# Optimization experiments

Hardware: AMD Instinct MI355X
Metric: run time of the kernel (lower is better)

Reference implementation:

```python
import jax, jax.numpy as jnp
import numpy as np
from math import ceil

N, C_IN, HV, WV = 4, 3, 256, 256
C, K, NUM_LAYERS = 16, 3, 10
HK, WK = 45, 45
PROX_SCALE, KSCALE, KBSCALE, EPS = 10.0, 100.0, 0.01, 1e-8


def conv2_same(x, w):
    # torch F.conv2d (cross-correlation) with 'same' padding
    return jax.lax.conv_general_dilated(x, w, (1, 1), 'SAME',
                                        dimension_numbers=('NCHW', 'OIHW', 'NCHW'))


def pad_to(x, size):
    h, w = x.shape[-2], x.shape[-1]
    pads = [(0, 0)] * (x.ndim - 2) + [(0, size[0] - h), (0, size[1] - w)]
    return jnp.pad(x, pads)


def soft_threshold(x, b):
    return jnp.sign(x) * jax.nn.relu(jnp.abs(x) - b)


def circ_shift(x, s):
    return jnp.roll(x, (-s[0], -s[1]), axis=(-2, -1))


def csq(c):
    return (c * jnp.conj(c)).real


def forward(blurred_image, w0, ws, biases, kernel_biases, kernel_proxes, zetas, eta):
    Nb, C_in, Hv, Wv = blurred_image.shape
    Hs, Ws = Hv + HK - 1, Wv + WK - 1
    Hb, Wb = Hs + HK - 1, Ws + WK - 1
    fft_size = (int(ceil(Hb / 64.0) * 64), int(ceil(Wb / 64.0) * 64))
    rfft = lambda x: jnp.fft.rfft2(x, s=fft_size, axes=(-2, -1))
    irfft = lambda X: jnp.fft.irfft2(X, s=fft_size, axes=(-2, -1))

    # first-layer filter: zero-mean per (out,in) filter, then spatial reflect
    w_mean = w0.reshape(C, C_in, -1).mean(axis=-1)
    w0c = w0 - w_mean[:, :, None, None]
    w0_unreflected = jnp.transpose(w0c, (1, 0, 2, 3))   # (C_in, C, K, K)
    w0r = w0c[:, :, ::-1, ::-1]

    # analysis: cascade of convs, each feature stack padded to fft_size
    wy_list = []
    fy = blurred_image
    for layer in range(NUM_LAYERS):
        w = w0r if layer == 0 else ws[layer - 1]
        fy = conv2_same(fy, w)
        fy_p = pad_to(jnp.pad(fy, ((0, 0), (0, 0), (HK - 1, HK - 1), (WK - 1, WK - 1))), fft_size)
        wy_list.append(fy_p)

    delta = jnp.zeros((Nb, HK, WK), dtype=blurred_image.dtype).at[:, HK // 2, WK // 2].set(1.0)
    b0 = biases[0][None, :, None, None]
    z = soft_threshold(circ_shift(wy_list[-1], (HK // 2, WK // 2)), b0)
    Fz = rfft(z)
    k = delta
    Fg = None
    for layer in range(NUM_LAYERS):
        fy_p = wy_list.pop()
        Ffy = rfft(fy_p)                       # (N, C, H, Wf) complex
        Fk = rfft(k)[:, None]                  # (N, 1, H, Wf)
        zeta = PROX_SCALE * zetas[layer][None, :, None, None]
        num = zeta * (jnp.conj(Fk) * Ffy) + Fz
        den = zeta * csq(Fk) + 1.0
        Fg = num / (den + EPS)
        b = biases[layer + 1][None, :, None, None]
        z = soft_threshold(irfft(Fg), b)
        Fz = rfft(z)
        zk = kernel_proxes[layer]
        num_k = zk * jnp.sum(jnp.conj(Fz) * Ffy, axis=1) + Fk[:, 0]
        den_k = zk * jnp.sum(csq(Fz), axis=1) + 1.0
        k = irfft(num_k / (den_k + EPS))
        k_flat = k.reshape(Nb, -1)
        k_max = jax.scipy.special.logsumexp(k_flat * KSCALE, axis=-1) / KSCALE
        bk = KBSCALE * kernel_biases[layer]
        k = jax.nn.relu(k[:, :HK, :WK] - bk * k_max[:, None, None])
        k_sum = jnp.sum(k, axis=(1, 2), keepdims=True)
        k = (k + EPS * delta) / (k_sum + EPS)

    # final closed-form image solve in frequency domain (3-channel Cramer's rule)
    Fy = rfft(jnp.pad(blurred_image, ((0, 0), (0, 0), (HK - 1, HK - 1), (WK - 1, WK - 1))))
    Fk = rfft(k)                                # (N, H, Wf)
    Fw0 = rfft(circ_shift(pad_to(w0_unreflected, fft_size), (K // 2, K // 2)))  # (C_in, C, H, Wf)
    b_final = biases[NUM_LAYERS + 1][None, :, None, None]
    Fg = rfft(soft_threshold(irfft(Fg), b_final))

    eta_s = PROX_SCALE * eta[None, :, None, None]      # (1, C, 1, 1)
    Fwr, Fwg, Fwb = Fw0[0:1], Fw0[1:2], Fw0[2:3]       # (1, C, H, Wf)
    Fyr, Fyg, Fyb = Fy[:, 0], Fy[:, 1], Fy[:, 2]
    Fk_sq = csq(Fk)
    Crr = Fk_sq + jnp.sum(eta_s * csq(Fwr), axis=1)
    Cgg = Fk_sq + jnp.sum(eta_s * csq(Fwg), axis=1)
    Cbb = Fk_sq + jnp.sum(eta_s * csq(Fwb), axis=1)
    Crg = jnp.sum(eta_s * jnp.conj(Fwr) * Fwg, axis=1)
    Crb = jnp.sum(eta_s * jnp.conj(Fwr) * Fwb, axis=1)
    Cgb = jnp.sum(eta_s * jnp.conj(Fwg) * Fwb, axis=1)
    Fk_conj = jnp.conj(Fk)
    Br = Fk_conj * Fyr + jnp.sum(eta_s * jnp.conj(Fwr) * Fg, axis=1)
    Bg = Fk_conj * Fyg + jnp.sum(eta_s * jnp.conj(Fwg) * Fg, axis=1)
    Bb = Fk_conj * Fyb + jnp.sum(eta_s * jnp.conj(Fwb) * Fg, axis=1)
    Crg_sq, Crb_sq, Cgb_sq = csq(Crg), csq(Crb), csq(Cgb)
    Irr = Cgg * Cbb - Cgb_sq
    Igg = Crr * Cbb - Crb_sq
    Ibb = Crr * Cgg - Crg_sq
    Irg = jnp.conj(Cgb) * Crb - Cbb * Crg
    Irb = Crg * Cgb - Cgg * Crb
    Igb = jnp.conj(Crg) * Crb - Crr * Cgb
    den = (Crr * (Cgg * Cbb - Cgb_sq) - Cgg * Crb_sq - Cbb * Crg_sq
           + 2 * (Crg * Cgb * jnp.conj(Crb)).real) + EPS
    Fxr = Irr * Br + Irg * Bg + Irb * Bb
    Fxg = jnp.conj(Irg) * Br + Igg * Bg + Igb * Bb
    Fxb = jnp.conj(Irb) * Br + jnp.conj(Igb) * Bg + Ibb * Bb
    Fx = jnp.stack([Fxr, Fxg, Fxb], axis=1) / den[:, None]

    image = irfft(Fx)[:, :, HK // 2:HK // 2 + Hv, WK // 2:WK // 2 + Wv]
    return image, k


def setup_inputs() -> dict:
    key = jax.random.key(0)
    ks = jax.random.split(key, 4)

    def xavier(k, shape, fan_in, fan_out):
        std = (2.0 / (fan_in + fan_out)) ** 0.5
        return std * jax.random.normal(k, shape, dtype=jnp.float32)

    return {
        'blurred_image': jax.random.normal(ks[0], (N, C_IN, HV, WV), dtype=jnp.float32),
        'w0': xavier(ks[1], (C, C_IN, K, K), C_IN * K * K, C * K * K),
        'ws': xavier(ks[2], (NUM_LAYERS - 1, C, C, 3, 3), C * 9, C * 9),
        'biases': jnp.full((NUM_LAYERS + 2, C), 0.02, dtype=jnp.float32),
        'kernel_biases': jnp.zeros((NUM_LAYERS,), dtype=jnp.float32),
        'kernel_proxes': jnp.ones((NUM_LAYERS,), dtype=jnp.float32),
        'zetas': jnp.ones((NUM_LAYERS, C), dtype=jnp.float32),
        'eta': jnp.ones((C,), dtype=jnp.float32),
    }


def reference(blurred_image, w0, ws, biases, kernel_biases, kernel_proxes, zetas, eta):
    return forward(blurred_image, w0, ws, biases, kernel_biases, kernel_proxes, zetas, eta)
```

## Files before the change

### kernel.cpp

```cpp
#include <hip/hip_runtime.h>
#include <math.h>

#define FH 384
#define KF 193
#define KS 384
#define SPW 147456

typedef __attribute__((ext_vector_type(8))) short short8;
typedef __attribute__((ext_vector_type(4))) float f32x4;
typedef unsigned int u32;
typedef unsigned short u16;

static __device__ __forceinline__ float softt(float v, float b) {
    return copysignf(fmaxf(fabsf(v) - b, 0.f), v);
}
static __device__ __forceinline__ u16 bf16_rn(float v) {
    u32 u = __float_as_uint(v);
    u32 r = (u + 0x7FFFu + ((u >> 16) & 1u)) >> 16;
    return (u16)r;
}
static __device__ __forceinline__ float bf16_to_f(u16 h) {
    return __uint_as_float(((u32)h) << 16);
}
static __device__ __forceinline__ float2 ldc(const uint2* __restrict__ S, size_t i) {
    uint2 u = S[i];
    float2 r;
    r.x = __uint_as_float((u.x & 0xffffu) << 16) + __uint_as_float((u.y & 0xffffu) << 16);
    r.y = __uint_as_float(u.x & 0xffff0000u) + __uint_as_float(u.y & 0xffff0000u);
    return r;
}
static __device__ __forceinline__ float2 ldcu(uint2 u) {
    float2 r;
    r.x = __uint_as_float((u.x & 0xffffu) << 16) + __uint_as_float((u.y & 0xffffu) << 16);
    r.y = __uint_as_float(u.x & 0xffff0000u) + __uint_as_float(u.y & 0xffff0000u);
    return r;
}
static __device__ __forceinline__ uint2 packc(float re, float im) {
    u16 hr = bf16_rn(re), hi = bf16_rn(im);
    u16 lr = bf16_rn(re - bf16_to_f(hr)), li = bf16_rn(im - bf16_to_f(hi));
    uint2 o; o.x = (u32)hr | ((u32)hi << 16); o.y = (u32)lr | ((u32)li << 16);
    return o;
}

__global__ void init_ef_k(float2* Ef) {
    int idx = blockIdx.x * 256 + threadIdx.x;
    if (idx >= FH * FH) return;
    int h = idx / FH, j = idx % FH;
    int m = (h * j) % FH;
    float th = (float)(6.283185307179586 / FH) * (float)m;
    float2 v; v.x = cosf(th); v.y = -sinf(th);
    Ef[idx] = v;
}

__global__ void init_tw(float2* twT) {
    int i = blockIdx.x * 256 + threadIdx.x;
    if (i < 193) {
        float th = (float)(6.283185307179586 / 384.0) * (float)i;
        float2 v; v.x = cosf(th); v.y = sinf(th);
        twT[i] = v;
    }
}

__global__ void init_estack192(u16* __restrict__ H, u16* __restrict__ L, int inv)
{
    int idx = blockIdx.x * 256 + threadIdx.x;
    if (idx >= KS * KS) return;
    int gm = idx / KS, kp = idx % KS;
    int m = gm >> 1, comp = gm & 1;
    int t = kp >> 1, ri = kp & 1;
    int mm = (m * t) % 192;
    float th = (float)(6.283185307179586 / 192.0) * (float)mm;
    float c = cosf(th), s = sinf(th);
    float er, ei;
    if (inv) { er = c * (1.f/384.f); ei = s * (1.f/384.f); }
    else     { er = c;               ei = -s; }
    float v;
    if (comp == 0) v = (ri == 0) ? er : -ei;
    else           v = (ri == 0) ? ei :  er;
    u16 h = bf16_rn(v);
    H[idx] = h;
    L[idx] = bf16_rn(v - bf16_to_f(h));
}

__global__ void init_t192(u16* __restrict__ H, u16* __restrict__ L)
{
    int idx = blockIdx.x * 256 + threadIdx.x;
    if (idx >= 208 * 192) return;
    int n = idx / 192, m = idx % 192;
    float v = 0.f;
    if (n < 194) {
        int j = n >> 1, ri = n & 1;
        int mm = (j * m) % 192;
        float th = (float)(6.283185307179586 / 192.0) * (float)mm;
        v = ri ? -sinf(th) : cosf(th);
    }
    u16 h = bf16_rn(v);
    H[idx] = h;
    L[idx] = bf16_rn(v - bf16_to_f(h));
}

__global__ void init_u192(u16* __restrict__ H, u16* __restrict__ L)
{
    int idx = blockIdx.x * 256 + threadIdx.x;
    if (idx >= 192 * 224) return;
    int m = idx / 224, kk = idx % 224;
    float v = 0.f;
    if (kk < 194) {
        int j = kk >> 1, ri = kk & 1;
        float cj = (j == 0 || j == 96) ? (1.f/384.f) : (2.f/384.f);
        int mm = (j * m) % 192;
        float th = (float)(6.283185307179586 / 192.0) * (float)mm;
        v = ri ? -cj*sinf(th) : cj*cosf(th);
    }
    u16 h = bf16_rn(v);
    H[idx] = h;
    L[idx] = bf16_rn(v - bf16_to_f(h));
}

__global__ void w0c_kernel(const float* __restrict__ w0, float* __restrict__ w0c) {
    int t = threadIdx.x;
    if (t < 48) {
        float m = 0.f;
        for (int d = 0; d < 9; ++d) m += w0[t*9+d];
        m *= (1.f/9.f);
        for (int d = 0; d < 9; ++d) w0c[t*9+d] = w0[t*9+d] - m;
    }
}

__global__ __launch_bounds__(256) void conv3x3_kernel(
    const float* __restrict__ inpF0, const u16* __restrict__ inH0, const u16* __restrict__ inL0,
    const float* __restrict__ w,
    u16* __restrict__ outH0, u16* __restrict__ outL0, int Cin, int flip,
    size_t inImgStride)
{
    size_t iofs = (size_t)blockIdx.z * inImgStride;
    const float* inF = inpF0 ? inpF0 + iofs : nullptr;
    const u16*   iH  = inH0 ? inH0 + iofs : nullptr;
    const u16*   iL  = inL0 ? inL0 + iofs : nullptr;
    u16* oH = outH0 + (size_t)blockIdx.z * 16*65536;
    u16* oL = outL0 + (size_t)blockIdx.z * 16*65536;
    __shared__ float tile[18][19];
    __shared__ float wl[16*16*9];
    int x0 = blockIdx.x * 16, y0 = blockIdx.y * 16;
    int t = threadIdx.x;
    int tx = t & 15, ty = t >> 4;
    int nw = 16 * Cin * 9;
    for (int i = t; i < nw; i += 256) {
        int d = i % 9;
        wl[i] = flip ? w[i + 8 - 2*d] : w[i];
    }
    float acc[16];
#pragma unroll
    for (int co = 0; co < 16; ++co) acc[co] = 0.f;
    for (int ci = 0; ci < Cin; ++ci) {
        __syncthreads();
        for (int i = t; i < 18*18; i += 256) {
            int yy = i / 18, xx = i % 18;
            int gy = y0 - 1 + yy, gx = x0 - 1 + xx;
            float v = 0.f;
            if (gy >= 0 && gy < 256 && gx >= 0 && gx < 256) {
                size_t ii;
                if (inF) ii = ((size_t)ci*256 + gy)*256 + gx;
                else     ii = ((size_t)ci*256 + gy)*256 + ((gx>>1) + (gx&1)*128);
                v = inF ? inF[ii] : (bf16_to_f(iH[ii]) + bf16_to_f(iL[ii]));
            }
            tile[yy][xx] = v;
        }
        __syncthreads();
        float v[9];
#pragma unroll
        for (int dy = 0; dy < 3; dy++)
#pragma unroll
            for (int dx = 0; dx < 3; dx++) v[dy*3+dx] = tile[ty+dy][tx+dx];
#pragma unroll
        for (int co = 0; co < 16; co++) {
            const float* wp = &wl[(co*Cin+ci)*9];
            acc[co] += v[0]*wp[0]+v[1]*wp[1]+v[2]*wp[2]
                     + v[3]*wp[3]+v[4]*wp[4]+v[5]*wp[5]
                     + v[6]*wp[6]+v[7]*wp[7]+v[8]*wp[8];
        }
    }
    int xo = x0 + tx;
    int xd = (xo >> 1) + (xo & 1)*128;
#pragma unroll
    for (int co = 0; co < 16; co++) {
        size_t o = ((size_t)co*256 + (y0+ty))*256 + xd;
        u16 h = bf16_rn(acc[co]);
        oH[o] = h;
        oL[o] = bf16_rn(acc[co] - bf16_to_f(h));
    }
}

__global__ void zinit_kernel(const u16* __restrict__ fy9H, const u16* __restrict__ fy9L,
                             const float* __restrict__ b0,
                             u16* __restrict__ oH, u16* __restrict__ oL, int total)
{
    int idx = blockIdx.x*256 + threadIdx.x;
    if (idx >= total) return;
    int x = idx % FH; int r = idx / FH; int y = r % FH; int plane = r / FH;
    int c = plane & 15;
    int Y = y + 22; if (Y >= FH) Y -= FH;
    int X = x + 22; if (X >= FH) X -= FH;
    int yy = Y - 44, xx = X - 44;
    float v = 0.f;
    if (yy >= 0 && yy < 256 && xx >= 0 && xx < 256) {
        size_t ii = ((size_t)plane*256 + yy)*256 + ((xx>>1) + (xx&1)*128);
        v = bf16_to_f(fy9H[ii]) + bf16_to_f(fy9L[ii]);
    }
    float s = softt(v, b0[c]);
    u16 h = bf16_rn(s);
    size_t d = (size_t)plane*SPW + (size_t)y*FH + ((x>>1) + (x&1)*192);
    oH[d] = h;
    oL[d] = bf16_rn(s - bf16_to_f(h));
}

static __device__ __forceinline__ void r2c192_epilogue(
    f32x4 accA[2][4], f32x4 accB[2][4],
    int col0, int njN, int y0, int wave, int lm, int lq,
    const float2* __restrict__ twT,
    uint2* __restrict__ outp, int B, int plane)
{
#pragma unroll
    for (int mi = 0; mi < 2; ++mi) {
#pragma unroll
// ... 230 lines not shown
    int idx = blockIdx.x*256 + threadIdx.x;
    if (idx >= rows * 97) return;
    int j = idx % 97;
    size_t b = (size_t)(idx / 97) * KF;
    if (j == 96) {
        float2 f = ldc(S, b + 96);
        S[b + 96] = packc(2.f*f.x, -2.f*f.y);
    } else {
        float2 f1 = ldc(S, b + j);
        float2 f2 = ldc(S, b + 192 - j);
        float gpx = f1.x + f2.x, gpy = f1.y - f2.y;
        float hx  = f1.x - f2.x, hy  = f1.y + f2.y;
        float2 tw = twT[j];
        float gmx = tw.x*hx - tw.y*hy;
        float gmy = tw.x*hy + tw.y*hx;
        S[b + j]       = packc(gpx, gpy);
        S[b + 192 - j] = packc(gmx, gmy);
    }
}

template<bool FUSE_LSE>
__global__ __launch_bounds__(256) void c2r192(
    const uint2* __restrict__ Ain,
    const u16* __restrict__ UH, const u16* __restrict__ UL,
    float* __restrict__ outp, const float* __restrict__ thr,
    u16* __restrict__ spH, u16* __restrict__ spL, int B,
    float2* __restrict__ parts)
{
    __shared__ u16 AhS[2][8*64*8];
    __shared__ u16 AlS[2][8*64*8];
    int col0 = blockIdx.x * 64;
    int y0   = blockIdx.y * 128;
    int plane = blockIdx.z;
    int tid = threadIdx.x;
    int wave = tid >> 6, lane = tid & 63;
    int lm = lane & 15, lq = lane >> 4;
    f32x4 accP[2][4], accQ[2][4];
#pragma unroll
    for (int mi = 0; mi < 2; ++mi)
#pragma unroll
        for (int nj = 0; nj < 4; ++nj) {
            accP[mi][nj] = (f32x4){0.f,0.f,0.f,0.f};
            accQ[mi][nj] = (f32x4){0.f,0.f,0.f,0.f};
        }
    for (int kt = 0; kt < 194; kt += 32) {
#pragma unroll
        for (int s = 0; s < 8; ++s) {
            int slot = tid + s*256;
            int p   = slot >> 10;
            int inr = slot & 1023;
            int r = inr >> 3, kq = inr & 7;
            size_t rowb = ((size_t)(y0 + r)*B + plane)*KF;
            int j0 = (kt + kq*4) >> 1;
            uint2 u0, u1;
            u0.x = u0.y = u1.x = u1.y = 0u;
            if (p == 0) {
                if (j0 < 96) u0 = Ain[rowb + j0];
                else if (j0 == 96) {
                    uint2 t = Ain[rowb + 96];
                    u0.x = t.x & 0xffffu; u0.y = t.y & 0xffffu;
                }
                if (j0 + 1 < 96) u1 = Ain[rowb + j0 + 1];
            } else {
                if (j0 < 96) u0 = Ain[rowb + 192 - j0];
                else if (j0 == 96) {
                    uint2 t = Ain[rowb + 96];
                    u0.x = t.x >> 16; u0.y = t.y >> 16;
                }
                if (j0 + 1 < 96) u1 = Ain[rowb + 191 - j0];
            }
            int base = ((r >> 4)*64 + (r & 15) + 16*(kq >> 1))*8 + (kq & 1)*4;
            uint2 hp, lp;
            hp.x = u0.x; hp.y = u1.x;
            lp.x = u0.y; lp.y = u1.y;
            *(uint2*)&AhS[p][base] = hp;
            *(uint2*)&AlS[p][base] = lp;
        }
        __syncthreads();
        short8 A0h[2], A0l[2], A1h[2], A1l[2];
#pragma unroll
        for (int mi = 0; mi < 2; ++mi) {
            int fo = ((wave*2 + mi)*64 + lane)*8;
            A0h[mi] = *(const short8*)&AhS[0][fo];
            A0l[mi] = *(const short8*)&AlS[0][fo];
            A1h[mi] = *(const short8*)&AhS[1][fo];
            A1l[mi] = *(const short8*)&AlS[1][fo];
        }
#pragma unroll
        for (int nj = 0; nj < 4; ++nj) {
            size_t toff = (size_t)(col0 + nj*16 + lm)*224 + kt + lq*8;
            short8 Bh = *(const short8*)(UH + toff);
            short8 Bl = *(const short8*)(UL + toff);
#pragma unroll
            for (int mi = 0; mi < 2; ++mi) {
                accP[mi][nj] = __builtin_amdgcn_mfma_f32_16x16x32_bf16(A0h[mi], Bh, accP[mi][nj], 0, 0, 0);
                accP[mi][nj] = __builtin_amdgcn_mfma_f32_16x16x32_bf16(A0h[mi], Bl, accP[mi][nj], 0, 0, 0);
                accP[mi][nj] = __builtin_amdgcn_mfma_f32_16x16x32_bf16(A0l[mi], Bh, accP[mi][nj], 0, 0, 0);
                accQ[mi][nj] = __builtin_amdgcn_mfma_f32_16x16x32_bf16(A1h[mi], Bh, accQ[mi][nj], 0, 0, 0);
                accQ[mi][nj] = __builtin_amdgcn_mfma_f32_16x16x32_bf16(A1h[mi], Bl, accQ[mi][nj], 0, 0, 0);
                accQ[mi][nj] = __builtin_amdgcn_mfma_f32_16x16x32_bf16(A1l[mi], Bh, accQ[mi][nj], 0, 0, 0);
            }
        }
        __syncthreads();
    }
    float bthr = thr ? thr[plane & 15] : 0.f;
    float lm_ = -1e30f, ls_ = 0.f;
#pragma unroll
    for (int mi = 0; mi < 2; ++mi) {
#pragma unroll
        for (int nj = 0; nj < 4; ++nj) {
            int m = col0 + nj*16 + lm;
#pragma unroll
            for (int rr = 0; rr < 4; ++rr) {
                int y = y0 + wave*32 + mi*16 + lq*4 + rr;
                float xe = accP[mi][nj][rr];
                float xo = accQ[mi][nj][rr];
                float2 o2; o2.x = xe; o2.y = xo;
                *(float2*)&outp[((size_t)plane*FH + y)*FH + 2*m] = o2;
                if (spH) {
                    float s0 = softt(xe, bthr), s1 = softt(xo, bthr);
                    u16 h0 = bf16_rn(s0), h1 = bf16_rn(s1);
                    u16 l0 = bf16_rn(s0 - bf16_to_f(h0)), l1 = bf16_rn(s1 - bf16_to_f(h1));
                    size_t d = (size_t)plane*SPW + (size_t)y*FH + m;
                    spH[d]       = h0; spL[d]       = l0;
                    spH[d + 192] = h1; spL[d + 192] = l1;
                }
                if (FUSE_LSE) {
                    lse_comb(lm_, ls_, 100.f*xe, 1.f);
                    lse_comb(lm_, ls_, 100.f*xo, 1.f);
                }
            }
        }
    }
    if (FUSE_LSE) {
        __shared__ float sm[256], ss[256];
        sm[tid] = lm_; ss[tid] = ls_;
        __syncthreads();
        for (int st = 128; st > 0; st >>= 1) {
            if (tid < st) {
                float mm = sm[tid], sc = ss[tid];
                lse_comb(mm, sc, sm[tid+st], ss[tid+st]);
                sm[tid] = mm; ss[tid] = sc;
            }
            __syncthreads();
        }
        if (tid == 0) {
            float2 o; o.x = sm[0]; o.y = ss[0];
            parts[plane*9 + blockIdx.y*3 + blockIdx.x] = o;
        }
    }
}

template<bool FUSE_FG>
__global__ __launch_bounds__(256) void zgemm_col_mfma2(
    const u16* __restrict__ EH, const u16* __restrict__ EL,
    const uint2* __restrict__ Bm, uint2* __restrict__ Cm, int N, float sgn,
    int ktHi, const float2* __restrict__ twT,
    uint2* __restrict__ FzFg, const uint2* __restrict__ FkB,
    const float* __restrict__ zet16, int GKF)
{
    __shared__ u16 BhS[2][4*64*8];
    __shared__ u16 BlS[2][4*64*8];
    int col0 = blockIdx.x * 64;
    int row0 = blockIdx.y * 128;
    int tid = threadIdx.x;
    int wave = tid >> 6, lane = tid & 63;
    int lm = lane & 15, lq = lane >> 4;
    f32x4 accE[2][4], accO[2][4];
#pragma unroll
    for (int mi = 0; mi < 2; ++mi)
#pragma unroll
        for (int nj = 0; nj < 4; ++nj) {
            accE[mi][nj] = (f32x4){0.f,0.f,0.f,0.f};
            accO[mi][nj] = (f32x4){0.f,0.f,0.f,0.f};
        }
    int arow0 = row0 + wave*32 + lm;
    for (int kt = 0; kt < ktHi; kt += 32) {
        int tbase = kt >> 1;
#pragma unroll
        for (int s = 0; s < 4; ++s) {
            int slot = tid + s*256;
            int p    = slot >> 9;
            int inr  = slot & 511;
            int pair = inr >> 6;
            int n    = inr & 63;
            int gn   = col0 + n;
            int t0   = tbase + pair*2;
            uint2 u0, u1;
            u0.x = u0.y = u1.x = u1.y = 0u;
            if (gn < N) {
                u0 = Bm[(size_t)(2*t0 + p)*N + gn];
                u1 = Bm[(size_t)(2*t0 + 2 + p)*N + gn];
            }
            int ntile = n >> 4, n0 = n & 15;
            int lrow  = (pair >> 1)*16 + n0;
            int base  = (ntile*64 + lrow)*8 + (pair & 1)*4;
            uint2 hp, lp;
            hp.x = u0.x; hp.y = u1.x;
            lp.x = u0.y; lp.y = u1.y;
            *(uint2*)&BhS[p][base] = hp;
            *(uint2*)&BlS[p][base] = lp;
        }
        __syncthreads();
        short8 Ah[2], Al[2];
#pragma unroll
        for (int mi = 0; mi < 2; ++mi) {
            size_t aoff = (size_t)(arow0 + mi*16)*KS + kt + lq*8;
            Ah[mi] = *(const short8*)(EH + aoff);
            Al[mi] = *(const short8*)(EL + aoff);
        }
#pragma unroll
        for (int nj = 0; nj < 4; ++nj) {
            short8 Bh0 = *(const short8*)&BhS[0][(nj*64 + lane)*8];
            short8 Bl0 = *(const short8*)&BlS[0][(nj*64 + lane)*8];
            short8 Bh1 = *(const short8*)&BhS[1][(nj*64 + lane)*8];
            short8 Bl1 = *(const short8*)&BlS[1][(nj*64 + lane)*8];
#pragma unroll
            for (int mi = 0; mi < 2; ++mi) {
                accE[mi][nj] = __builtin_amdgcn_mfma_f32_16x16x32_bf16(Ah[mi], Bh0, accE[mi][nj], 0, 0, 0);
                accE[mi][nj] = __builtin_amdgcn_mfma_f32_16x16x32_bf16(Ah[mi], Bl0, accE[mi][nj], 0, 0, 0);
                accE[mi][nj] = __builtin_amdgcn_mfma_f32_16x16x32_bf16(Al[mi], Bh0, accE[mi][nj], 0, 0, 0);
                accO[mi][nj] = __builtin_amdgcn_mfma_f32_16x16x32_bf16(Ah[mi], Bh1, accO[mi][nj], 0, 0, 0);
                accO[mi][nj] = __builtin_amdgcn_mfma_f32_16x16x32_bf16(Ah[mi], Bl1, accO[mi][nj], 0, 0, 0);
                accO[mi][nj] = __builtin_amdgcn_mfma_f32_16x16x32_bf16(Al[mi], Bh1, accO[mi][nj], 0, 0, 0);
            }
        }
        __syncthreads();
    }
#pragma unroll
    for (int mi = 0; mi < 2; ++mi) {
#pragma unroll
        for (int nj = 0; nj < 4; ++nj) {
            int coln = col0 + nj*16 + lm;
            if (coln < N) {
                int r0 = row0 + wave*32 + mi*16 + lq*4;
                int h  = r0 >> 1;
                int kk = 0, imgI = 0;
                float zeta = 0.f;
                if (FUSE_FG) {
                    int planeI = coln / KF;
                    kk = coln - planeI*KF;
                    imgI = planeI >> 4;
                    zeta = 10.f * zet16[planeI & 15];
                }
#pragma unroll
                for (int pp = 0; pp < 2; ++pp) {
                    float e_re = accE[mi][nj][2*pp],   e_im = accE[mi][nj][2*pp+1];
                    float o_re = accO[mi][nj][2*pp],   o_im = accO[mi][nj][2*pp+1];
                    int hh = h + pp;
                    float2 tw = twT[hh];
                    float twr = tw.x, twi = sgn * tw.y;
                    float tr = twr*o_re - twi*o_im;
                    float ti = twr*o_im + twi*o_re;
                    uint2 pa = packc(e_re + tr, e_im + ti);
                    uint2 pb = packc(e_re - tr, e_im - ti);
                    Cm[(size_t)hh*N + coln]         = pa;
                    Cm[(size_t)(hh + 192)*N + coln] = pb;
                    if (FUSE_FG) {
#pragma unroll
                        for (int e = 0; e < 2; ++e) {
                            int row = hh + e*192;
                            float2 fy = ldcu(e ? pb : pa);
                            float2 fz = ldc(FzFg, (size_t)row*N + coln);
                            float2 fk = ldc(FkB, (size_t)row*GKF + imgI*KF + kk);
                            float nx = zeta*(fk.x*fy.x + fk.y*fy.y) + fz.x;
                            float ny = zeta*(fk.x*fy.y - fk.y*fy.x) + fz.y;
                            float den = zeta*(fk.x*fk.x + fk.y*fk.y) + 1.f + 1e-8f;
                            float inv = 1.f/den;
                            FzFg[(size_t)row*N + coln] = packc(nx*inv, ny*inv);
                        }
                    }
                }
            }
        }
    }
}

__global__ void knum_kernel(const uint2* __restrict__ Fz, const uint2* __restrict__ Ffy,
                            const uint2* __restrict__ Fk, const float* __restrict__ kprox,
                            int L, int total, uint2* __restrict__ outk)
{
    int idx = blockIdx.x*256 + threadIdx.x;
    if (idx >= total) return;
    int k = idx % KF; int r = idx / KF;
    float zk = kprox[L];
    float s1x = 0.f, s1y = 0.f, s2 = 0.f;
    for (int c = 0; c < 16; ++c) {
        size_t bi = ((size_t)r*16 + c)*KF + k;
        float2 fz = ldc(Fz, bi), fy = ldc(Ffy, bi);
        s1x += fz.x*fy.x + fz.y*fy.y;
        s1y += fz.x*fy.y - fz.y*fy.x;
        s2  += fz.x*fz.x + fz.y*fz.y;
    }
    float2 fk = ldc(Fk, idx);
    float nx = zk*s1x + fk.x, ny = zk*s1y + fk.y;
    float den = zk*s2 + 1.f + 1e-8f;
    float inv = 1.f/den;
    outk[idx] = packc(nx*inv, ny*inv);
}

__global__ void zero_kernel(float* __restrict__ p, int n)
{
    int i = blockIdx.x*256 + threadIdx.x;
    if (i < n) p[i] = 0.f;
}

__global__ void kdelta_kernel(float* __restrict__ kful, int G)
{
    int t = threadIdx.x;
    if (t < G) kful[(size_t)t*FH*FH + 22*FH + 22] = 1.f;
}

__global__ __launch_bounds__(256) void knew_kernel(const float2* __restrict__ parts,
    const float* __restrict__ kraw0, const float* __restrict__ kb, int L,
    float* __restrict__ kful0)
{
    int img = blockIdx.x;
    const float* kraw = kraw0 + (size_t)img*FH*FH;
    float*       kful = kful0 + (size_t)img*FH*FH;
    int t = threadIdx.x;
    __shared__ float sm[16], ss[16];
    if (t < 16) {
        if (t < 9) { float2 p = parts[img*9 + t]; sm[t] = p.x; ss[t] = p.y; }
        else       { sm[t] = -1e30f; ss[t] = 0.f; }
    }
    __syncthreads();
    for (int st = 8; st > 0; st >>= 1) {
        if (t < st) {
            float mm = sm[t], sc = ss[t];
            lse_comb(mm, sc, sm[t+st], ss[t+st]);
            sm[t] = mm; ss[t] = sc;
        }
        __syncthreads();
    }
    float kmax = (sm[0] + logf(ss[0])) * 0.01f;
    float thr = 0.01f * kb[L] * kmax;
    float vs[8]; float loc = 0.f;
#pragma unroll
    for (int ii = 0; ii < 8; ++ii) {
        int i = t + ii*256;
        float v = 0.f;
        if (i < 45*45) {
            int y = i/45, x = i - y*45;
            v = fmaxf(kraw[y*FH + x] - thr, 0.f);
        }
        vs[ii] = v; loc += v;
    }
    __shared__ float sr[256];
    sr[t] = loc; __syncthreads();
    for (int st = 128; st > 0; st >>= 1) { if (t < st) sr[t] += sr[t+st]; __syncthreads(); }
    float den = sr[0] + 1e-8f;
#pragma unroll
    for (int ii = 0; ii < 8; ++ii) {
        int i = t + ii*256;
        if (i < 45*45) {
            int y = i/45, x = i - y*45;
            float v = vs[ii] + ((y == 22 && x == 22) ? 1e-8f : 0.f);
            kful[y*FH + x] = v / den;
        }
    }
}

__global__ void fw0_kernel(const float* __restrict__ w0c, const float2* __restrict__ Ef,
                           float2* __restrict__ Fw0)
{
    int idx = blockIdx.x*256 + threadIdx.x;
    if (idx >= 48*FH*KF) return;
    int k = idx % KF; int r = idx / KF;
    int c = r & 15; int r2 = r >> 4;
    int ci = r2 % 3; int h = r2 / 3;
    float accx = 0.f, accy = 0.f;
#pragma unroll
    for (int ky = 0; ky < 3; ++ky) {
        int a1 = ky - 1; if (a1 < 0) a1 += FH;
        float2 e1 = Ef[h*FH + a1];
#pragma unroll
        for (int kx = 0; kx < 3; ++kx) {
            int a2 = kx - 1; if (a2 < 0) a2 += FH;
            float2 e2 = Ef[k*FH + a2];
            float wv = w0c[((c*3 + ci)*3 + ky)*3 + kx];
            float tr = e1.x*e2.x - e1.y*e2.y;
            float ti = e1.x*e2.y + e1.y*e2.x;
            accx += wv*tr; accy += wv*ti;
        }
    }
    float2 o; o.x = accx; o.y = accy;
    Fw0[idx] = o;
}

__global__ void wiener_kernel(const uint2* __restrict__ Fk, const uint2* __restrict__ Fy,
    const float2* __restrict__ Fw0, const uint2* __restrict__ Fg2,
    const float* __restrict__ eta, int G, int total, uint2* __restrict__ Fx)
{
    int idx = blockIdx.x*256 + threadIdx.x;
    if (idx >= total) return;
    int k = idx % KF; int r = idx / KF;
    int h = r / G;
    float2 fk = ldc(Fk, idx);
    float fksq = fk.x*fk.x + fk.y*fk.y;
    float2 fyr = ldc(Fy, ((size_t)3*r + 0)*KF + k);
    float2 fyg = ldc(Fy, ((size_t)3*r + 1)*KF + k);
    float2 fyb = ldc(Fy, ((size_t)3*r + 2)*KF + k);
    float Crr = fksq, Cgg = fksq, Cbb = fksq;
    float2 Crg, Crb, Cgb;
    Crg.x = Crg.y = Crb.x = Crb.y = Cgb.x = Cgb.y = 0.f;
    float2 Br, Bg, Bb;
    Br.x = fk.x*fyr.x + fk.y*fyr.y; Br.y = fk.x*fyr.y - fk.y*fyr.x;
    Bg.x = fk.x*fyg.x + fk.y*fyg.y; Bg.y = fk.x*fyg.y - fk.y*fyg.x;
    Bb.x = fk.x*fyb.x + fk.y*fyb.y; Bb.y = fk.x*fyb.y - fk.y*fyb.x;
    for (int c = 0; c < 16; ++c) {
        float es = 10.f * eta[c];
        float2 wr = Fw0[((size_t)h*48 +  0 + c)*KF + k];
        float2 wg = Fw0[((size_t)h*48 + 16 + c)*KF + k];
        float2 wb = Fw0[((size_t)h*48 + 32 + c)*KF + k];
        float2 g  = ldc(Fg2, ((size_t)r*16 + c)*KF + k);
        Crr += es*(wr.x*wr.x + wr.y*wr.y);
        Cgg += es*(wg.x*wg.x + wg.y*wg.y);
        Cbb += es*(wb.x*wb.x + wb.y*wb.y);
        Crg.x += es*(wr.x*wg.x + wr.y*wg.y); Crg.y += es*(wr.x*wg.y - wr.y*wg.x);
        Crb.x += es*(wr.x*wb.x + wr.y*wb.y); Crb.y += es*(wr.x*wb.y - wr.y*wb.x);
        Cgb.x += es*(wg.x*wb.x + wg.y*wb.y); Cgb.y += es*(wg.x*wb.y - wg.y*wb.x);
        Br.x += es*(wr.x*g.x + wr.y*g.y); Br.y += es*(wr.x*g.y - wr.y*g.x);
        Bg.x += es*(wg.x*g.x + wg.y*g.y); Bg.y += es*(wg.x*g.y - wg.y*g.x);
        Bb.x += es*(wb.x*g.x + wb.y*g.y); Bb.y += es*(wb.x*g.y - wb.y*g.x);
    }
    float Crg_sq = Crg.x*Crg.x + Crg.y*Crg.y;
    float Crb_sq = Crb.x*Crb.x + Crb.y*Crb.y;
    float Cgb_sq = Cgb.x*Cgb.x + Cgb.y*Cgb.y;
    float Irr = Cgg*Cbb - Cgb_sq;
    float Igg = Crr*Cbb - Crb_sq;
    float Ibb = Crr*Cgg - Crg_sq;
    float2 Irg, Irb, Igb;
    Irg.x = (Cgb.x*Crb.x + Cgb.y*Crb.y) - Cbb*Crg.x;
    Irg.y = (Cgb.x*Crb.y - Cgb.y*Crb.x) - Cbb*Crg.y;
    Irb.x = (Crg.x*Cgb.x - Crg.y*Cgb.y) - Cgg*Crb.x;
    Irb.y = (Crg.x*Cgb.y + Crg.y*Cgb.x) - Cgg*Crb.y;
    Igb.x = (Crg.x*Crb.x + Crg.y*Crb.y) - Crr*Cgb.x;
    Igb.y = (Crg.x*Crb.y - Crg.y*Crb.x) - Crr*Cgb.y;
    float tx_ = Crg.x*Cgb.x - Crg.y*Cgb.y;
    float ty_ = Crg.x*Cgb.y + Crg.y*Cgb.x;
    float den = Crr*Irr - Cgg*Crb_sq - Cbb*Crg_sq + 2.f*(tx_*Crb.x + ty_*Crb.y) + 1e-8f;
    float inv = 1.f/den;
    float ox, oy;
    ox = (Irr*Br.x + (Irg.x*Bg.x - Irg.y*Bg.y) + (Irb.x*Bb.x - Irb.y*Bb.y))*inv;
    oy = (Irr*Br.y + (Irg.x*Bg.y + Irg.y*Bg.x) + (Irb.x*Bb.y + Irb.y*Bb.x))*inv;
    Fx[((size_t)3*r + 0)*KF + k] = packc(ox, oy);
    ox = ((Irg.x*Br.x + Irg.y*Br.y) + Igg*Bg.x + (Igb.x*Bb.x - Igb.y*Bb.y))*inv;
    oy = ((Irg.x*Br.y - Irg.y*Br.x) + Igg*Bg.y + (Igb.x*Bb.y + Igb.y*Bb.x))*inv;
    Fx[((size_t)3*r + 1)*KF + k] = packc(ox, oy);
    ox = ((Irb.x*Br.x + Irb.y*Br.y) + (Igb.x*Bg.x + Igb.y*Bg.y) + Ibb*Bb.x)*inv;
    oy = ((Irb.x*Br.y - Irb.y*Br.x) + (Igb.x*Bg.y - Igb.y*Bg.x) + Ibb*Bb.y)*inv;
    Fx[((size_t)3*r + 2)*KF + k] = packc(ox, oy);
}

__global__ void crop_kernel(const float* __restrict__ sp, float* __restrict__ outp, int total)
{
    int idx = blockIdx.x*256 + threadIdx.x;
    if (idx >= total) return;
    int x = idx & 255; int r = idx >> 8; int y = r & 255; int plane = r >> 8;
    outp[idx] = sp[((size_t)plane*FH + (y+22))*FH + (x+22)];
}

__global__ void kcopy_kernel(const float* __restrict__ kful, float* __restrict__ outp, int total)
{
    int idx = blockIdx.x*256 + threadIdx.x;
    if (idx >= total) return;
    int rem = idx % 2025; int img = idx / 2025;
    int x = rem % 45; int y = rem / 45;
    outp[idx] = kful[(size_t)img*FH*FH + y*FH + x];
}

extern "C" void kernel_launch(void* const* d_in, const int* in_sizes, int n_in,
                              void* d_out, int out_size, void* d_ws, size_t ws_size,
                              hipStream_t stream)
{
    (void)in_sizes; (void)n_in; (void)out_size;
    const float* blurred = (const float*)d_in[0];
    const float* w0      = (const float*)d_in[1];
    const float* wsw     = (const float*)d_in[2];
    const float* biases  = (const float*)d_in[3];
    const float* kbias   = (const float*)d_in[4];
    const float* kprox   = (const float*)d_in[5];
    const float* zetas   = (const float*)d_in[6];
    const float* eta     = (const float*)d_in[7];
    float* outp = (float*)d_out;

    auto al = [](size_t b) { return (b + 255) & ~(size_t)255; };
    auto need = [&](int G) -> size_t {
        size_t s = 0;
        s += al((size_t)FH*FH*8);
        s += al(193*8);
        s += 4*al((size_t)KS*KS*2);
        s += 2*al((size_t)208*192*2);
        s += 2*al((size_t)192*224*2);
        s += al(432*4);
        s += 2*al((size_t)10*G*16*65536*2);
        s += al((size_t)G*16*FH*FH*4);
        s += 2*al((size_t)G*16*SPW*2);
        s += 3*al((size_t)G*16*FH*KF*8);
        s += 4*al((size_t)G*FH*KF*8);
        s += 2*al((size_t)G*FH*FH*4);
        s += 2*al((size_t)G*3*FH*KF*8);
        s += al((size_t)G*64*8);
        return s;
    };
    int G = 4;
    while (G > 1 && need(G) > ws_size) G >>= 1;

    char* base = (char*)d_ws;
    size_t off = 0;
    auto alloc = [&](size_t bytes) -> void* {
        void* p = (void*)(base + off);
        off += (bytes + 255) & ~(size_t)255;
        return p;
    };
    float2* Ef   = (float2*)alloc((size_t)FH*FH*8);
    float2* twT  = (float2*)alloc(193*8);
    u16* EfH = (u16*)alloc((size_t)KS*KS*2);
    u16* EfL = (u16*)alloc((size_t)KS*KS*2);
    u16* EiH = (u16*)alloc((size_t)KS*KS*2);
    u16* EiL = (u16*)alloc((size_t)KS*KS*2);
    u16* T1H = (u16*)alloc((size_t)208*192*2);
    u16* T1L = (u16*)alloc((size_t)208*192*2);
    u16* U1H = (u16*)alloc((size_t)192*224*2);
    u16* U1L = (u16*)alloc((size_t)192*224*2);
    float*  w0cB = (float*)alloc(432*4);
    u16*    fyH  = (u16*)alloc((size_t)10*G*16*65536*2);
    u16*    fyL  = (u16*)alloc((size_t)10*G*16*65536*2);
    float*  zsp  = (float*)alloc((size_t)G*16*FH*FH*4);
    u16*    zspSH= (u16*)alloc((size_t)G*16*SPW*2);
    u16*    zspSL= (u16*)alloc((size_t)G*16*SPW*2);
    uint2*  mid  = (uint2*)alloc((size_t)G*16*FH*KF*8);
    uint2*  FzFg = (uint2*)alloc((size_t)G*16*FH*KF*8);
    uint2*  Ffy  = (uint2*)alloc((size_t)G*16*FH*KF*8);
    uint2*  Fk   = (uint2*)alloc((size_t)G*FH*KF*8);
    uint2*  kfA  = (uint2*)alloc((size_t)G*FH*KF*8);
    uint2*  kfB  = (uint2*)alloc((size_t)G*FH*KF*8);
    uint2*  kmid = (uint2*)alloc((size_t)G*FH*KF*8);
    float*  kraw = (float*)alloc((size_t)G*FH*FH*4);
    float*  kful = (float*)alloc((size_t)G*FH*FH*4);
    uint2*  FyB  = (uint2*)alloc((size_t)G*3*FH*KF*8);
    uint2*  FxB  = (uint2*)alloc((size_t)G*3*FH*KF*8);
    float2* lseP = (float2*)alloc((size_t)G*64*8);
    float2* Fw0B = (float2*)fyH;

    init_ef_k<<<(FH*FH+255)/256, 256, 0, stream>>>(Ef);
    init_tw<<<1, 256, 0, stream>>>(twT);
    init_estack192<<<(KS*KS+255)/256, 256, 0, stream>>>(EfH, EfL, 0);
    init_estack192<<<(KS*KS+255)/256, 256, 0, stream>>>(EiH, EiL, 1);
    init_t192<<<(208*192+255)/256, 256, 0, stream>>>(T1H, T1L);
    init_u192<<<(192*224+255)/256, 256, 0, stream>>>(U1H, U1L);
    w0c_kernel<<<1, 64, 0, stream>>>(w0, w0cB);

    auto zgf = [&](const uint2* Bm, uint2* Cm, int Ncols) {
        zgemm_col_mfma2<false><<<dim3((Ncols+63)/64, 3), 256, 0, stream>>>(
            EfH, EfL, Bm, Cm, Ncols, -1.f, KS, twT, nullptr, nullptr, nullptr, 0);
    };
    auto zgi = [&](const uint2* Bm, uint2* Cm, int Ncols) {
        zgemm_col_mfma2<false><<<dim3((Ncols+63)/64, 3), 256, 0, stream>>>(
            EiH, EiL, Bm, Cm, Ncols, 1.f, KS, twT, nullptr, nullptr, nullptr, 0);
    };
    auto r2c = [&](const float* inp, int inH, int inW, int oY, int oX,
                   const float* thr, uint2* o, int B) {
        r2c192_f<<<dim3(4, 3, B), 256, 0, stream>>>(
            inp, inH, inW, inW, (size_t)inH*inW, oY, oX, thr, T1H, T1L, twT, o, B);
    };
    auto r2cs = [&](const u16* Hs, const u16* Ls, int inH, int inW, int oY, int oX,
                    uint2* o, int B) {
        r2c192_s<<<dim3(4, 3, B), 256, 0, stream>>>(
            Hs, Ls, inH, inW, oY, oX, T1H, T1L, twT, o, B);
    };
    auto c2r = [&](uint2* Ain, float* o, int B,
                   const float* thr, u16* sH, u16* sL) {
        int rows = FH * B;
        gpm_kernel<<<(rows*97 + 255)/256, 256, 0, stream>>>(Ain, twT, rows);
        c2r192<false><<<dim3(3, 3, B), 256, 0, stream>>>(
            Ain, U1H, U1L, o, thr, sH, sL, B, nullptr);
    };
    auto c2rk = [&](uint2* Ain, float* o, int B, float2* parts) {
        int rows = FH * B;
        gpm_kernel<<<(rows*97 + 255)/256, 256, 0, stream>>>(Ain, twT, rows);
        c2r192<true><<<dim3(3, 3, B), 256, 0, stream>>>(
            Ain, U1H, U1L, o, nullptr, nullptr, nullptr, B, parts);
    };
    auto r2ck = [&]() {
        r2c192_f<<<dim3(4, 1, G), 256, 0, stream>>>(
            kful, 45, 45, FH, (size_t)FH*FH, 0, 0, nullptr, T1H, T1L, twT, kmid, G);
        zgemm_col_mfma2<false><<<dim3((G*KF+63)/64, 3), 256, 0, stream>>>(
            EfH, EfL, kmid, Fk, G*KF, -1.f, 64, twT, nullptr, nullptr, nullptr, 0);
    };

    const size_t CKL = (size_t)G*16*65536;

    for (int g0 = 0; g0 < 4; g0 += G) {
        const float* img = blurred + (size_t)g0*3*65536;

        conv3x3_kernel<<<dim3(16,16,G), 256, 0, stream>>>(
            img, nullptr, nullptr, w0cB, fyH, fyL, 3, 1, (size_t)3*65536);
        for (int l = 1; l < 10; ++l)
            conv3x3_kernel<<<dim3(16,16,G), 256, 0, stream>>>(
                nullptr, fyH + (size_t)(l-1)*CKL, fyL + (size_t)(l-1)*CKL,
                wsw + (size_t)(l-1)*2304,
                fyH + (size_t)l*CKL, fyL + (size_t)l*CKL, 16, 0, (size_t)16*65536);

        int totZ = G*16*FH*FH;
        zinit_kernel<<<(totZ+255)/256, 256, 0, stream>>>(
            fyH + 9*CKL, fyL + 9*CKL, biases, zspSH, zspSL, totZ);
        r2cs(zspSH, zspSL, FH, FH, 0, 0, mid, G*16);
        zgf(mid, FzFg, G*16*KF);

        zero_kernel<<<(G*FH*FH+255)/256, 256, 0, stream>>>(kful, G*FH*FH);
        kdelta_kernel<<<1, 64, 0, stream>>>(kful, G);

        int totK = G*FH*KF;
        int NS = G*16*KF;
        for (int it = 0; it < 10; ++it) {
            int Lfy = 9 - it;
            r2ck();
            r2cs(fyH + (size_t)Lfy*CKL, fyL + (size_t)Lfy*CKL, 256, 256, 44, 44, mid, G*16);
            zgemm_col_mfma2<true><<<dim3((NS+63)/64, 3), 256, 0, stream>>>(
                EfH, EfL, mid, Ffy, NS, -1.f, KS, twT,
                FzFg, Fk, zetas + it*16, G*KF);
            zgi(FzFg, mid, NS);
            c2r(mid, zsp, G*16, biases + (it+1)*16, zspSH, zspSL);
            r2cs(zspSH, zspSL, FH, FH, 0, 0, mid, G*16);
            zgf(mid, FzFg, NS);
            knum_kernel<<<(totK+255)/256, 256, 0, stream>>>(FzFg, Ffy, Fk, kprox, it, totK, kfA);
            zgi(kfA, kfB, G*KF);
            c2rk(kfB, kraw, G, lseP);
            knew_kernel<<<G, 256, 0, stream>>>(lseP, kraw, kbias, it, kful);
        }

        r2c(img, 256, 256, 44, 44, nullptr, mid, 3*G);
        zgf(mid, FyB, 3*G*KF);
        r2ck();
        r2c(zsp, FH, FH, 0, 0, biases + 11*16, mid, G*16);
        zgf(mid, FzFg, G*16*KF);
        fw0_kernel<<<(48*FH*KF+255)/256, 256, 0, stream>>>(w0cB, Ef, Fw0B);
        wiener_kernel<<<(totK+255)/256, 256, 0, stream>>>(Fk, FyB, Fw0B, FzFg, eta, G, totK, FxB);
        zgi(FxB, mid, 3*G*KF);
        c2r(mid, zsp, 3*G, nullptr, nullptr, nullptr);
        int totC = G*3*65536;
        crop_kernel<<<(totC+255)/256, 256, 0, stream>>>(zsp, outp + (size_t)g0*3*65536, totC);
        int totKC = G*2025;
        kcopy_kernel<<<(totKC+255)/256, 256, 0, stream>>>(kful, outp + 786432 + g0*2025, totKC);
    }
}
```

Measured before the change: 8.775 ms.

## Replace radix-2 split with radix-4 decomposition in column DFT GEMM

The column-direction 384-point DFT was computed as two 192-point DFT GEMMs (even/odd rows) followed by a radix-2 butterfly. It now runs four 96-point DFT GEMMs over the stride-4 row subsets, followed by a radix-4 butterfly with twiddles w, w^2, w^3 in the epilogue. This shrinks the DFT matrix and the GEMM K dimension, cutting MFMA work and matrix-operand traffic. The cost is a larger LDS B buffer, a heavier epilogue, and extra twiddle products computed in fp32 that could affect accuracy slightly.

```diff
diff --git a/kernel.cpp b/kernel.cpp
--- a/kernel.cpp
+++ b/kernel.cpp
@@ -3,7 +3,6 @@
 
 #define FH 384
 #define KF 193
-#define KS 384
 #define SPW 147456
 
 typedef __attribute__((ext_vector_type(8))) short short8;
@@ -40,6 +39,9 @@
     u16 lr = bf16_rn(re - bf16_to_f(hr)), li = bf16_rn(im - bf16_to_f(hi));
     uint2 o; o.x = (u32)hr | ((u32)hi << 16); o.y = (u32)lr | ((u32)li << 16);
     return o;
+}
+static __device__ __forceinline__ float2 cmul(float2 a, float2 b) {
+    float2 r; r.x = a.x*b.x - a.y*b.y; r.y = a.x*b.y + a.y*b.x; return r;
 }
 
 __global__ void init_ef_k(float2* Ef) {
@@ -61,15 +63,15 @@
     }
 }
 
-__global__ void init_estack192(u16* __restrict__ H, u16* __restrict__ L, int inv)
+__global__ void init_e96(u16* __restrict__ H, u16* __restrict__ L, int inv)
 {
     int idx = blockIdx.x * 256 + threadIdx.x;
-    if (idx >= KS * KS) return;
-    int gm = idx / KS, kp = idx % KS;
+    if (idx >= 192 * 192) return;
+    int gm = idx / 192, kp = idx % 192;
     int m = gm >> 1, comp = gm & 1;
     int t = kp >> 1, ri = kp & 1;
-    int mm = (m * t) % 192;
-    float th = (float)(6.283185307179586 / 192.0) * (float)mm;
+    int mm = (m * t) % 96;
+    float th = (float)(6.283185307179586 / 96.0) * (float)mm;
     float c = cosf(th), s = sinf(th);
     float er, ei;
     if (inv) { er = c * (1.f/384.f); ei = s * (1.f/384.f); }
@@ -606,33 +608,31 @@
 }
 
 template<bool FUSE_FG>
-__global__ __launch_bounds__(256) void zgemm_col_mfma2(
+__global__ __launch_bounds__(256) void zgemm_col_mfma4(
     const u16* __restrict__ EH, const u16* __restrict__ EL,
     const uint2* __restrict__ Bm, uint2* __restrict__ Cm, int N, float sgn,
     int ktHi, const float2* __restrict__ twT,
     uint2* __restrict__ FzFg, const uint2* __restrict__ FkB,
     const float* __restrict__ zet16, int GKF)
 {
-    __shared__ u16 BhS[2][4*64*8];
-    __shared__ u16 BlS[2][4*64*8];
+    __shared__ u16 BhS[4][4*64*8];
+    __shared__ u16 BlS[4][4*64*8];
     int col0 = blockIdx.x * 64;
-    int row0 = blockIdx.y * 128;
+    int row0 = blockIdx.y * 64;
     int tid = threadIdx.x;
     int wave = tid >> 6, lane = tid & 63;
     int lm = lane & 15, lq = lane >> 4;
-    f32x4 accE[2][4], accO[2][4];
-#pragma unroll
-    for (int mi = 0; mi < 2; ++mi)
-#pragma unroll
-        for (int nj = 0; nj < 4; ++nj) {
-            accE[mi][nj] = (f32x4){0.f,0.f,0.f,0.f};
-            accO[mi][nj] = (f32x4){0.f,0.f,0.f,0.f};
-        }
-    int arow0 = row0 + wave*32 + lm;
+    f32x4 acc[4][4];
+#pragma unroll
+    for (int p = 0; p < 4; ++p)
+#pragma unroll
+        for (int nj = 0; nj < 4; ++nj)
+            acc[p][nj] = (f32x4){0.f,0.f,0.f,0.f};
+    int arow = row0 + wave*16 + lm;
     for (int kt = 0; kt < ktHi; kt += 32) {
         int tbase = kt >> 1;
 #pragma unroll
-        for (int s = 0; s < 4; ++s) {
+        for (int s = 0; s < 8; ++s) {
             int slot = tid + s*256;
             int p    = slot >> 9;
             int inr  = slot & 511;
@@ -643,8 +643,8 @@
             uint2 u0, u1;
             u0.x = u0.y = u1.x = u1.y = 0u;
             if (gn < N) {
-                u0 = Bm[(size_t)(2*t0 + p)*N + gn];
-                u1 = Bm[(size_t)(2*t0 + 2 + p)*N + gn];
+                u0 = Bm[(size_t)(4*t0 + p)*N + gn];
+                u1 = Bm[(size_t)(4*t0 + 4 + p)*N + gn];
             }
             int ntile = n >> 4, n0 = n & 15;
             int lrow  = (pair >> 1)*16 + n0;
@@ -656,73 +656,78 @@
             *(uint2*)&BlS[p][base] = lp;
         }
         __syncthreads();
-        short8 Ah[2], Al[2];
-#pragma unroll
-        for (int mi = 0; mi < 2; ++mi) {
-            size_t aoff = (size_t)(arow0 + mi*16)*KS + kt + lq*8;
-            Ah[mi] = *(const short8*)(EH + aoff);
-            Al[mi] = *(const short8*)(EL + aoff);
+        short8 Ah, Al;
+        {
+            size_t aoff = (size_t)arow*192 + kt + lq*8;
+            Ah = *(const short8*)(EH + aoff);
+            Al = *(const short8*)(EL + aoff);
         }
 #pragma unroll
         for (int nj = 0; nj < 4; ++nj) {
-            short8 Bh0 = *(const short8*)&BhS[0][(nj*64 + lane)*8];
-            short8 Bl0 = *(const short8*)&BlS[0][(nj*64 + lane)*8];
-            short8 Bh1 = *(const short8*)&BhS[1][(nj*64 + lane)*8];
-            short8 Bl1 = *(const short8*)&BlS[1][(nj*64 + lane)*8];
-#pragma unroll
-            for (int mi = 0; mi < 2; ++mi) {
-                accE[mi][nj] = __builtin_amdgcn_mfma_f32_16x16x32_bf16(Ah[mi], Bh0, accE[mi][nj], 0, 0, 0);
-                accE[mi][nj] = __builtin_amdgcn_mfma_f32_16x16x32_bf16(Ah[mi], Bl0, accE[mi][nj], 0, 0, 0);
-                accE[mi][nj] = __builtin_amdgcn_mfma_f32_16x16x32_bf16(Al[mi], Bh0, accE[mi][nj], 0, 0, 0);
-                accO[mi][nj] = __builtin_amdgcn_mfma_f32_16x16x32_bf16(Ah[mi], Bh1, accO[mi][nj], 0, 0, 0);
-                accO[mi][nj] = __builtin_amdgcn_mfma_f32_16x16x32_bf16(Ah[mi], Bl1, accO[mi][nj], 0, 0, 0);
-                accO[mi][nj] = __builtin_amdgcn_mfma_f32_16x16x32_bf16(Al[mi], Bh1, accO[mi][nj], 0, 0, 0);
+#pragma unroll
+            for (int p = 0; p < 4; ++p) {
+                short8 Bh = *(const short8*)&BhS[p][(nj*64 + lane)*8];
+                short8 Bl = *(const short8*)&BlS[p][(nj*64 + lane)*8];
+                acc[p][nj] = __builtin_amdgcn_mfma_f32_16x16x32_bf16(Ah, Bh, acc[p][nj], 0, 0, 0);
+                acc[p][nj] = __builtin_amdgcn_mfma_f32_16x16x32_bf16(Ah, Bl, acc[p][nj], 0, 0, 0);
+                acc[p][nj] = __builtin_amdgcn_mfma_f32_16x16x32_bf16(Al, Bh, acc[p][nj], 0, 0, 0);
             }
         }
         __syncthreads();
     }
 #pragma unroll
-    for (int mi = 0; mi < 2; ++mi) {
-#pragma unroll
-        for (int nj = 0; nj < 4; ++nj) {
-            int coln = col0 + nj*16 + lm;
-            if (coln < N) {
-                int r0 = row0 + wave*32 + mi*16 + lq*4;
-                int h  = r0 >> 1;
-                int kk = 0, imgI = 0;
-                float zeta = 0.f;
-                if (FUSE_FG) {
-                    int planeI = coln / KF;
-                    kk = coln - planeI*KF;
-                    imgI = planeI >> 4;
-                    zeta = 10.f * zet16[planeI & 15];
-                }
-#pragma unroll
-                for (int pp = 0; pp < 2; ++pp) {
-                    float e_re = accE[mi][nj][2*pp],   e_im = accE[mi][nj][2*pp+1];
-                    float o_re = accO[mi][nj][2*pp],   o_im = accO[mi][nj][2*pp+1];
-                    int hh = h + pp;
-                    float2 tw = twT[hh];
-                    float twr = tw.x, twi = sgn * tw.y;
-                    float tr = twr*o_re - twi*o_im;
-                    float ti = twr*o_im + twi*o_re;
-                    uint2 pa = packc(e_re + tr, e_im + ti);
-                    uint2 pb = packc(e_re - tr, e_im - ti);
-                    Cm[(size_t)hh*N + coln]         = pa;
-                    Cm[(size_t)(hh + 192)*N + coln] = pb;
+    for (int nj = 0; nj < 4; ++nj) {
+        int coln = col0 + nj*16 + lm;
+        if (coln < N) {
+            int r0 = row0 + wave*16 + lq*4;
+            int h0b = r0 >> 1;
+            int kk = 0, imgI = 0;
+            float zeta = 0.f;
+            if (FUSE_FG) {
+                int planeI = coln / KF;
+                kk = coln - planeI*KF;
+                imgI = planeI >> 4;
+                zeta = 10.f * zet16[planeI & 15];
+            }
+#pragma unroll
+            for (int pp = 0; pp < 2; ++pp) {
+                int h0 = h0b + pp;
+                float2 c0, c1, c2, c3;
+                c0.x = acc[0][nj][2*pp]; c0.y = acc[0][nj][2*pp+1];
+                c1.x = acc[1][nj][2*pp]; c1.y = acc[1][nj][2*pp+1];
+                c2.x = acc[2][nj][2*pp]; c2.y = acc[2][nj][2*pp+1];
+                c3.x = acc[3][nj][2*pp]; c3.y = acc[3][nj][2*pp+1];
+                float2 w1; { float2 t = twT[h0]; w1.x = t.x; w1.y = sgn*t.y; }
+                float2 w2 = cmul(w1, w1);
+                float2 w3 = cmul(w2, w1);
+                float2 d1 = cmul(c1, w1);
+                float2 d2 = cmul(c2, w2);
+                float2 d3 = cmul(c3, w3);
+                float2 s02, m02, s13, m13, i13;
+                s02.x = c0.x + d2.x; s02.y = c0.y + d2.y;
+                m02.x = c0.x - d2.x; m02.y = c0.y - d2.y;
+                s13.x = d1.x + d3.x; s13.y = d1.y + d3.y;
+                m13.x = d1.x - d3.x; m13.y = d1.y - d3.y;
+                i13.x = -sgn*m13.y;  i13.y = sgn*m13.x;
+                float2 X[4];
+                X[0].x = s02.x + s13.x; X[0].y = s02.y + s13.y;
+                X[2].x = s02.x - s13.x; X[2].y = s02.y - s13.y;
+                X[1].x = m02.x + i13.x; X[1].y = m02.y + i13.y;
+                X[3].x = m02.x - i13.x; X[3].y = m02.y - i13.y;
+#pragma unroll
+                for (int q = 0; q < 4; ++q) {
+                    int row = h0 + 96*q;
+                    uint2 px = packc(X[q].x, X[q].y);
+                    Cm[(size_t)row*N + coln] = px;
                     if (FUSE_FG) {
-#pragma unroll
-                        for (int e = 0; e < 2; ++e) {
-                            int row = hh + e*192;
-                            float2 fy = ldcu(e ? pb : pa);
-                            float2 fz = ldc(FzFg, (size_t)row*N + coln);
-                            float2 fk = ldc(FkB, (size_t)row*GKF + imgI*KF + kk);
-                            float nx = zeta*(fk.x*fy.x + fk.y*fy.y) + fz.x;
-                            float ny = zeta*(fk.x*fy.y - fk.y*fy.x) + fz.y;
-                            float den = zeta*(fk.x*fk.x + fk.y*fk.y) + 1.f + 1e-8f;
-                            float inv = 1.f/den;
-                            FzFg[(size_t)row*N + coln] = packc(nx*inv, ny*inv);
-                        }
+                        float2 fy = ldcu(px);
+                        float2 fz = ldc(FzFg, (size_t)row*N + coln);
+                        float2 fk = ldc(FkB, (size_t)row*GKF + imgI*KF + kk);
+                        float nx = zeta*(fk.x*fy.x + fk.y*fy.y) + fz.x;
+                        float ny = zeta*(fk.x*fy.y - fk.y*fy.x) + fz.y;
+                        float den = zeta*(fk.x*fk.x + fk.y*fk.y) + 1.f + 1e-8f;
+                        float inv = 1.f/den;
+                        FzFg[(size_t)row*N + coln] = packc(nx*inv, ny*inv);
                     }
                 }
             }
@@ -944,7 +949,7 @@
         size_t s = 0;
         s += al((size_t)FH*FH*8);
         s += al(193*8);
-        s += 4*al((size_t)KS*KS*2);
+        s += 4*al((size_t)192*192*2);
         s += 2*al((size_t)208*192*2);
         s += 2*al((size_t)192*224*2);
         s += al(432*4);
@@ -970,10 +975,10 @@
     };
     float2* Ef   = (float2*)alloc((size_t)FH*FH*8);
     float2* twT  = (float2*)alloc(193*8);
-    u16* EfH = (u16*)alloc((size_t)KS*KS*2);
-    u16* EfL = (u16*)alloc((size_t)KS*KS*2);
-    u16* EiH = (u16*)alloc((size_t)KS*KS*2);
-    u16* EiL = (u16*)alloc((size_t)KS*KS*2);
+    u16* EfH = (u16*)alloc((size_t)192*192*2);
+    u16* EfL = (u16*)alloc((size_t)192*192*2);
+    u16* EiH = (u16*)alloc((size_t)192*192*2);
+    u16* EiL = (u16*)alloc((size_t)192*192*2);
     u16* T1H = (u16*)alloc((size_t)208*192*2);
     u16* T1L = (u16*)alloc((size_t)208*192*2);
     u16* U1H = (u16*)alloc((size_t)192*224*2);
@@ -1000,19 +1005,19 @@
 
     init_ef_k<<<(FH*FH+255)/256, 256, 0, stream>>>(Ef);
     init_tw<<<1, 256, 0, stream>>>(twT);
-    init_estack192<<<(KS*KS+255)/256, 256, 0, stream>>>(EfH, EfL, 0);
-    init_estack192<<<(KS*KS+255)/256, 256, 0, stream>>>(EiH, EiL, 1);
+    init_e96<<<(192*192+255)/256, 256, 0, stream>>>(EfH, EfL, 0);
+    init_e96<<<(192*192+255)/256, 256, 0, stream>>>(EiH, EiL, 1);
     init_t192<<<(208*192+255)/256, 256, 0, stream>>>(T1H, T1L);
     init_u192<<<(192*224+255)/256, 256, 0, stream>>>(U1H, U1L);
     w0c_kernel<<<1, 64, 0, stream>>>(w0, w0cB);
 
     auto zgf = [&](const uint2* Bm, uint2* Cm, int Ncols) {
-        zgemm_col_mfma2<false><<<dim3((Ncols+63)/64, 3), 256, 0, stream>>>(
-            EfH, EfL, Bm, Cm, Ncols, -1.f, KS, twT, nullptr, nullptr, nullptr, 0);
+        zgemm_col_mfma4<false><<<dim3((Ncols+63)/64, 3), 256, 0, stream>>>(
+            EfH, EfL, Bm, Cm, Ncols, -1.f, 192, twT, nullptr, nullptr, nullptr, 0);
     };
     auto zgi = [&](const uint2* Bm, uint2* Cm, int Ncols) {
-        zgemm_col_mfma2<false><<<dim3((Ncols+63)/64, 3), 256, 0, stream>>>(
-            EiH, EiL, Bm, Cm, Ncols, 1.f, KS, twT, nullptr, nullptr, nullptr, 0);
+        zgemm_col_mfma4<false><<<dim3((Ncols+63)/64, 3), 256, 0, stream>>>(
+            EiH, EiL, Bm, Cm, Ncols, 1.f, 192, twT, nullptr, nullptr, nullptr, 0);
     };
     auto r2c = [&](const float* inp, int inH, int inW, int oY, int oX,
                    const float* thr, uint2* o, int B) {
@@ -1040,8 +1045,8 @@
     auto r2ck = [&]() {
         r2c192_f<<<dim3(4, 1, G), 256, 0, stream>>>(
             kful, 45, 45, FH, (size_t)FH*FH, 0, 0, nullptr, T1H, T1L, twT, kmid, G);
-        zgemm_col_mfma2<false><<<dim3((G*KF+63)/64, 3), 256, 0, stream>>>(
-            EfH, EfL, kmid, Fk, G*KF, -1.f, 64, twT, nullptr, nullptr, nullptr, 0);
+        zgemm_col_mfma4<false><<<dim3((G*KF+63)/64, 3), 256, 0, stream>>>(
+            EfH, EfL, kmid, Fk, G*KF, -1.f, 32, twT, nullptr, nullptr, nullptr, 0);
     };
 
     const size_t CKL = (size_t)G*16*65536;
@@ -1072,8 +1077,8 @@
             int Lfy = 9 - it;
             r2ck();
             r2cs(fyH + (size_t)Lfy*CKL, fyL + (size_t)Lfy*CKL, 256, 256, 44, 44, mid, G*16);
-            zgemm_col_mfma2<true><<<dim3((NS+63)/64, 3), 256, 0, stream>>>(
-                EfH, EfL, mid, Ffy, NS, -1.f, KS, twT,
+            zgemm_col_mfma4<true><<<dim3((NS+63)/64, 3), 256, 0, stream>>>(
+                EfH, EfL, mid, Ffy, NS, -1.f, 192, twT,
                 FzFg, Fk, zetas + it*16, G*KF);
             zgi(FzFg, mid, NS);
             c2r(mid, zsp, G*16, biases + (it+1)*16, zspSH, zspSL);
```

After: 8.136 ms. -7.3%, faster.
